# Kernel optimization log

Hardware: AMD Instinct MI355X
Metric: run time of the kernel (lower is better)

The kernel has to match this reference:

```python
import jax, jax.numpy as jnp
import numpy as np

D_MODEL = 1024

def setup_inputs() -> dict:
    key = jax.random.key(0)
    ks = jax.random.split(key, 7)
    B, S, D = 4, 2048, D_MODEL
    scale = 1.0 / np.sqrt(D)
    x = jax.random.normal(ks[0], (B, S, D), dtype=jnp.float32)
    Wq = jax.random.normal(ks[1], (D, D), dtype=jnp.float32) * scale
    bq = jnp.zeros((D,), dtype=jnp.float32)
    Wk = jax.random.normal(ks[2], (D, D), dtype=jnp.float32) * scale
    bk = jnp.zeros((D,), dtype=jnp.float32)
    Wv = jax.random.normal(ks[3], (D, D), dtype=jnp.float32) * scale
    bv = jnp.zeros((D,), dtype=jnp.float32)
    return {"x": x, "Wq": Wq, "bq": bq, "Wk": Wk, "bk": bk, "Wv": Wv, "bv": bv}

def reference(x, Wq, bq, Wk, bk, Wv, bv):
    # Single-head attention; scale = 1/sqrt(d_model) as in the torch module (self.d_k = d_model).
    d_k = x.shape[-1]
    q = jnp.einsum('bsd,de->bse', x, Wq) + bq
    k = jnp.einsum('bsd,de->bse', x, Wk) + bk
    v = jnp.einsum('bsd,de->bse', x, Wv) + bv
    scores = jnp.einsum('bqd,bkd->bqk', q, k) / jnp.sqrt(jnp.asarray(d_k, x.dtype))
    attn = jax.nn.softmax(scores, axis=-1)
    return jnp.einsum('bqk,bkd->bqd', attn, v)
```

## Files before the change

kernel.cpp:

```cpp
#include <hip/hip_runtime.h>
#include <hip/hip_bf16.h>

#define DM 1024
#define SEQ 2048
#define NBATCH 4

using f32x4 = __attribute__((ext_vector_type(4))) float;
using s16x8 = __attribute__((ext_vector_type(8))) short;
using u16x4 = __attribute__((ext_vector_type(4))) unsigned short;
using u16x8 = __attribute__((ext_vector_type(8))) unsigned short;

__device__ __forceinline__ unsigned short f2bf(float f) {
  union { float f; unsigned u; } v; v.f = f;
  return (unsigned short)((v.u + 0x7fffu + ((v.u >> 16) & 1u)) >> 16);
}

__global__ void prep_k(const float* __restrict__ X,
                       const float* __restrict__ Wq, const float* __restrict__ Wk,
                       const float* __restrict__ Wv,
                       unsigned short* __restrict__ XB, unsigned short* __restrict__ WT) {
  __shared__ float t[32][33];
  const int b = blockIdx.x;
  if (b < 4096) {
    const int i = b * 256 + threadIdx.x;
    const f32x4* p = (const f32x4*)X;
    f32x4 a = p[2 * i], c = p[2 * i + 1];
    u16x8 o;
#pragma unroll
    for (int q = 0; q < 4; q++) { o[q] = f2bf(a[q]); o[4 + q] = f2bf(c[q]); }
    *(u16x8*)(XB + (size_t)i * 8) = o;
  } else {
    const int r2 = b - 4096;
    const int seg = r2 >> 10;
    const int rem = r2 & 1023;
    const int k0 = (rem >> 5) * 32, n0 = (rem & 31) * 32;
    const float* W = (seg == 0) ? Wq : (seg == 1) ? Wk : Wv;
    unsigned short* out = WT + (size_t)seg * DM * DM;
    const int tr = threadIdx.x >> 5, tc = threadIdx.x & 31;
#pragma unroll
    for (int p = 0; p < 4; p++) {
      int r = tr + p * 8;
      t[r][tc] = W[(size_t)(k0 + r) * DM + n0 + tc];
    }
    __syncthreads();
#pragma unroll
    for (int p = 0; p < 4; p++) {
      int r = tr + p * 8;
      out[(size_t)(n0 + r) * DM + k0 + tc] = f2bf(t[tc][r]);
    }
  }
}

template <int MODE, int BM, int LDA, int LDB, int KDIM>
__global__ void gemm_nt(const unsigned short* __restrict__ A,
                        const unsigned short* __restrict__ B,
                        void* __restrict__ C0,
                        unsigned short* __restrict__ C1,
                        unsigned short* __restrict__ C2,
                        const float* __restrict__ bq,
                        const float* __restrict__ bk,
                        const float* __restrict__ bv,
                        float* __restrict__ sm,
                        float* __restrict__ sv,
                        const float* __restrict__ Tt) {
  constexpr int ASTEPS = BM / 32;
  constexpr int NJ = (BM == 128) ? 4 : 2;
  constexpr int WNOFF = 16 * NJ;
  __shared__ unsigned short lbuf[(BM + 128) * 64];
  __shared__ float fred[256];
  __shared__ float Tl[(MODE == 2) ? 1024 : 1];

  const int tid = threadIdx.x;
  const int w = tid >> 6;
  const int L = tid & 63;
  const int wm = (BM == 128) ? (w & 1) : 0;
  const int wn = (BM == 128) ? (w >> 1) : w;
  const int qd = L >> 4, ll = L & 15;

  const int bid = blockIdx.x;
  const int xcd = bid & 7, slot = bid >> 3;
  int bz, tileM, tileN, nT;
  if (MODE == 0) {
    const int pm = xcd & 3, pn = xcd >> 2;
    const int nloc = slot % 12, mloc = slot / 12;
    bz = 0; tileM = (pm * 16 + mloc) * 128; tileN = (pn * 12 + nloc) * 128; nT = 0;
  } else if (MODE == 1) {
    bz = xcd >> 1;
    const int mh = xcd & 1;
    const int nloc = slot & 15, mloc = slot >> 4;
    tileM = (mh * 8 + mloc) * 128; tileN = nloc * 128; nT = nloc;
  } else {
    bz = xcd >> 1;
    const int mh = xcd & 1;
    const int nloc = slot & 7, mloc = slot >> 3;
    tileM = (mh * 16 + mloc) * 64; tileN = nloc * 128; nT = nloc;
  }
  (void)nT;

  const unsigned short* Ab = A;
  const unsigned short* Bb = B;
  if (MODE == 1) { Ab += (size_t)bz * SEQ * DM; Bb += (size_t)bz * SEQ * DM; }
  if (MODE == 2) { Ab += (size_t)bz * SEQ * SEQ; Bb += (size_t)bz * DM * SEQ; }

  const int srow = tid >> 3;
  const int pch = tid & 7;
  const int gch = pch ^ (srow & 7);
  const unsigned short* gA = Ab + (size_t)(tileM + srow) * LDA + gch * 8;
  const unsigned short* gB = Bb + (size_t)(tileN + srow) * LDB + gch * 8;
  unsigned short* lA = lbuf;
  unsigned short* lB = lbuf + BM * 64;
  unsigned short* wAp = &lA[srow * 64 + pch * 8];
  unsigned short* wBp = &lB[srow * 64 + pch * 8];

  u16x8 rA[ASTEPS], rB[4];
#define LOADT(kt) do {                                                         \
    const size_t kk_ = (size_t)(kt) * 64;                                      \
    _Pragma("unroll")                                                          \
    for (int i_ = 0; i_ < ASTEPS; i_++)                                        \
      rA[i_] = *(const u16x8*)(gA + (size_t)i_ * 32 * LDA + kk_);              \
    _Pragma("unroll")                                                          \
    for (int i_ = 0; i_ < 4; i_++)                                             \
      rB[i_] = *(const u16x8*)(gB + (size_t)i_ * 32 * LDB + kk_);              \
  } while (0)
#define WRITET() do {                                                          \
    _Pragma("unroll")                                                          \
    for (int i_ = 0; i_ < ASTEPS; i_++) *(u16x8*)(wAp + i_ * 32 * 64) = rA[i_];\
    _Pragma("unroll")                                                          \
    for (int i_ = 0; i_ < 4; i_++)      *(u16x8*)(wBp + i_ * 32 * 64) = rB[i_];\
  } while (0)

  f32x4 acc[4][NJ];
#pragma unroll
  for (int i = 0; i < 4; i++)
#pragma unroll
    for (int j = 0; j < NJ; j++) acc[i][j] = (f32x4){0.f, 0.f, 0.f, 0.f};

  const int sw = L & 7;

  constexpr int NK = KDIM / 64;
  LOADT(0);

  if (MODE == 2 && tid < 64) {
    const size_t rbase = (size_t)bz * SEQ + tileM + tid;
    const float* mrow = sm + rbase * 16;
    const float* srow2 = sv + rbase * 32;
    float mv[16];
#pragma unroll
    for (int t = 0; t < 16; t++) mv[t] = mrow[t];
    float M = mv[0];
#pragma unroll
    for (int t = 1; t < 16; t++) M = fmaxf(M, mv[t]);
    float Lsum = 0.f;
#pragma unroll
    for (int t = 0; t < 16; t++) Lsum += (srow2[2 * t] + srow2[2 * t + 1]) * __expf(mv[t] - M);
#pragma unroll
    for (int t = 1; t < 16; t++) Tl[(t - 1) * 64 + tid] = __expf(mv[t - 1] - mv[t]);
    Tl[15 * 64 + tid] = __expf(mv[15] - M) / Lsum;
  }

  WRITET();
  __syncthreads();

  float tTn[4][4];
  if (MODE == 2) {
#pragma unroll
    for (int i = 0; i < 4; i++)
#pragma unroll
      for (int r = 0; r < 4; r++) tTn[i][r] = Tl[i * 16 + qd * 4 + r];
  }

  for (int k = 0; k < NK; ++k) {
    if (MODE == 2 && k >= 2 && (k & 1) == 0) {
#pragma unroll
      for (int i = 0; i < 4; i++)
#pragma unroll
        for (int j = 0; j < NJ; j++)
#pragma unroll
          for (int r = 0; r < 4; r++) acc[i][j][r] *= tTn[i][r];
      const int tn = (k >> 1) + 1;
#pragma unroll
      for (int i = 0; i < 4; i++)
#pragma unroll
        for (int r = 0; r < 4; r++) tTn[i][r] = Tl[(tn - 1) * 64 + i * 16 + qd * 4 + r];
    }

    if (k + 1 < NK) LOADT(k + 1);

#pragma unroll
    for (int s = 0; s < 2; s++) {
      const int pc = ((s * 4 + qd) ^ sw) * 8;
      s16x8 av[4], bv4[NJ];
#pragma unroll
      for (int i = 0; i < 4; i++)
        av[i] = *(const s16x8*)&lA[(wm * 64 + i * 16 + ll) * 64 + pc];
#pragma unroll
      for (int j = 0; j < NJ; j++)
        bv4[j] = *(const s16x8*)&lB[(wn * WNOFF + j * 16 + ll) * 64 + pc];
#pragma unroll
      for (int i = 0; i < 4; i++)
#pragma unroll
        for (int j = 0; j < NJ; j++)
          acc[i][j] = __builtin_amdgcn_mfma_f32_16x16x32_bf16(av[i], bv4[j], acc[i][j], 0, 0, 0);
    }

    if (k + 1 < NK) {
      __builtin_amdgcn_s_waitcnt(0xC07F);
      __builtin_amdgcn_sched_barrier(0);
      __builtin_amdgcn_s_barrier();
      __builtin_amdgcn_sched_barrier(0);
      WRITET();
      __syncthreads();
    }
  }
#undef LOADT
#undef WRITET

  if (MODE == 0) {
#pragma unroll
    for (int i = 0; i < 4; i++) {
      const int gm0 = tileM + wm * 64 + i * 16 + qd * 4;
#pragma unroll
      for (int j = 0; j < NJ; j++) {
        const int gn = tileN + wn * WNOFF + j * 16 + ll;
        const int seg = gn >> 10;
        const int colin = gn & 1023;
        if (seg == 0) {
          const float bias = bq[colin];
          unsigned short* Q = (unsigned short*)C0;
#pragma unroll
          for (int r = 0; r < 4; r++) Q[(size_t)(gm0 + r) * DM + colin] = f2bf(acc[i][j][r] + bias);
        } else if (seg == 1) {
          const float bias = bk[colin];
#pragma unroll
          for (int r = 0; r < 4; r++) C1[(size_t)(gm0 + r) * DM + colin] = f2bf(acc[i][j][r] + bias);
        } else {
          const float bias = bv[colin];
          u16x4 pk;
#pragma unroll
          for (int r = 0; r < 4; r++) pk[r] = f2bf(acc[i][j][r] + bias);
          const int b = gm0 >> 11, s0 = gm0 & 2047;
          *(u16x4*)(C2 + ((size_t)((b << 10) + colin)) * SEQ + s0) = pk;
        }
      }
    }
  } else if (MODE == 1) {
    __syncthreads();
    float mt[4][4];
#pragma unroll
    for (int i = 0; i < 4; i++)
#pragma unroll
      for (int r = 0; r < 4; r++) {
#pragma unroll
        for (int j = 0; j < NJ; j++) acc[i][j][r] *= 0.03125f;
        float v = fmaxf(fmaxf(acc[i][0][r], acc[i][1][r]), fmaxf(acc[i][2][r], acc[i][3][r]));
#pragma unroll
        for (int m = 1; m < 16; m <<= 1) v = fmaxf(v, __shfl_xor(v, m, 16));
        mt[i][r] = v;
      }
    if (ll == 0) {
#pragma unroll
      for (int i = 0; i < 4; i++)
#pragma unroll
        for (int r = 0; r < 4; r++)
          fred[wn * 128 + wm * 64 + i * 16 + qd * 4 + r] = mt[i][r];
    }
    __syncthreads();
#pragma unroll
    for (int i = 0; i < 4; i++)
#pragma unroll
      for (int r = 0; r < 4; r++) {
        const int row = wm * 64 + i * 16 + qd * 4 + r;
        mt[i][r] = fmaxf(fred[row], fred[128 + row]);
      }
#pragma unroll
    for (int i = 0; i < 4; i++)
#pragma unroll
      for (int r = 0; r < 4; r++) {
        const int row = wm * 64 + i * 16 + qd * 4 + r;
        float s = 0.f;
#pragma unroll
        for (int j = 0; j < NJ; j++) {
          float e = __expf(acc[i][j][r] - mt[i][r]);
          s += e;
          const int col = wn * WNOFF + j * 16 + ll;
          lbuf[row * 128 + ((((col >> 4) ^ (row & 7)) << 4) | (col & 15))] = f2bf(e);
        }
#pragma unroll
        for (int m = 1; m < 16; m <<= 1) s += __shfl_xor(s, m, 16);
        if (ll == 0) {
          const size_t base = (size_t)bz * SEQ + tileM + row;
          sv[base * 32 + nT * 2 + wn] = s;
          if (wn == 0) sm[base * 16 + nT] = mt[i][r];
        }
      }
    __syncthreads();
    unsigned short* P = (unsigned short*)C0 + (size_t)bz * SEQ * SEQ;
#pragma unroll
    for (int p = 0; p < 8; p++) {
      const int c = p * 256 + tid;
      const int row = c >> 4, cg = c & 15;
      const int phys = ((((cg >> 1) ^ (row & 7)) << 4) | ((cg & 1) << 3));
      u16x8 val = *(const u16x8*)&lbuf[row * 128 + phys];
      *(u16x8*)(P + (size_t)(tileM + row) * SEQ + tileN + cg * 8) = val;
    }
  } else {
    float* O = (float*)C0 + (size_t)bz * SEQ * DM;
#pragma unroll
    for (int i = 0; i < 4; i++) {
      const int gm0 = tileM + i * 16 + qd * 4;
#pragma unroll
      for (int j = 0; j < NJ; j++) {
        const int gn = tileN + wn * WNOFF + j * 16 + ll;
#pragma unroll
        for (int r = 0; r < 4; r++)
          O[(size_t)(gm0 + r) * DM + gn] = acc[i][j][r] * tTn[i][r];
      }
    }
  }
  (void)Tt;
}

extern "C" void kernel_launch(void* const* d_in, const int* in_sizes, int n_in,
                              void* d_out, int out_size, void* d_ws, size_t ws_size,
                              hipStream_t stream) {
  (void)in_sizes; (void)n_in; (void)out_size; (void)ws_size;
  const float* x  = (const float*)d_in[0];
  const float* Wq = (const float*)d_in[1];
  const float* bq = (const float*)d_in[2];
  const float* Wk = (const float*)d_in[3];
  const float* bk = (const float*)d_in[4];
  const float* Wv = (const float*)d_in[5];
  const float* bv = (const float*)d_in[6];
  float* out = (float*)d_out;
  char* ws = (char*)d_ws;
  unsigned short* xb = (unsigned short*)(ws + 0);
  unsigned short* wt = (unsigned short*)(ws + 16777216);
  unsigned short* qb = (unsigned short*)(ws + 23068672);
  unsigned short* kb = (unsigned short*)(ws + 39845888);
  unsigned short* vt = (unsigned short*)(ws + 56623104);
  unsigned short* P  = (unsigned short*)(ws + 73400320);
  float*          ms = (float*)(ws + 106954752);
  float*          ss = (float*)(ws + 107479040);

  prep_k<<<7168, 256, 0, stream>>>(x, Wq, Wk, Wv, xb, wt);
  gemm_nt<0, 128, 1024, 1024, 1024><<<1536, 256, 0, stream>>>(
      xb, wt, (void*)qb, kb, vt, bq, bk, bv, nullptr, nullptr, nullptr);
  gemm_nt<1, 128, 1024, 1024, 1024><<<1024, 256, 0, stream>>>(
      qb, kb, (void*)P, nullptr, nullptr, nullptr, nullptr, nullptr, ms, ss, nullptr);
  gemm_nt<2, 64, 2048, 2048, 2048><<<1024, 256, 0, stream>>>(
      P, vt, (void*)out, nullptr, nullptr, nullptr, nullptr, nullptr, ms, ss, nullptr);
}
```

Before: 253.1 us.

## Replace QK^T scores GEMM with 256x256-tile kernel using direct global-to-LDS loads

Adds a dedicated scores kernel with 256x256 output tiles and 8 waves. It stages Q/K tiles straight into LDS via global_load_lds in a double-buffered pipeline with explicit barriers, waitcnts and priority hints. The per-tile softmax statistics change from 16 to 8 column tiles, and the PV GEMM's rescale schedule is updated to match. The aim is more data reuse per tile and overlap of loads with MFMA work, but there are only 256 blocks and P is now written with scattered 2-byte stores instead of staged vector stores.

```diff
diff --git a/kernel.cpp b/kernel.cpp
--- a/kernel.cpp
+++ b/kernel.cpp
@@ -13,6 +13,12 @@
 __device__ __forceinline__ unsigned short f2bf(float f) {
   union { float f; unsigned u; } v; v.f = f;
   return (unsigned short)((v.u + 0x7fffu + ((v.u >> 16) & 1u)) >> 16);
+}
+
+__device__ __forceinline__ void gll16(const unsigned short* g, unsigned short* l) {
+  __builtin_amdgcn_global_load_lds((const __attribute__((address_space(1))) void*)g,
+                                   (__attribute__((address_space(3))) void*)l,
+                                   16, 0, 0);
 }
 
 __global__ void prep_k(const float* __restrict__ X,
@@ -49,6 +55,171 @@
       out[(size_t)(n0 + r) * DM + k0 + tc] = f2bf(t[tc][r]);
     }
   }
+}
+
+__global__ __launch_bounds__(512, 2) void sgemm256_k(
+    const unsigned short* __restrict__ Qb,
+    const unsigned short* __restrict__ Kb,
+    unsigned short* __restrict__ P,
+    float* __restrict__ sm,
+    float* __restrict__ sv) {
+  __shared__ unsigned short lbuf[65536];
+  __shared__ float fred[1024];
+
+  const int tid = threadIdx.x;
+  const int w = tid >> 6, l = tid & 63;
+  const int ll = l & 15, qd = l >> 4;
+  const int wm = w >> 2, wn = w & 3;
+
+  const int bid = blockIdx.x;
+  const int xcd = bid & 7, slot = bid >> 3;
+  const int bz = xcd >> 1;
+  const int mh = xcd & 1;
+  const int nloc = slot & 7, mloc = slot >> 3;
+  const int tileM = (mh * 4 + mloc) * 256, tileN = nloc * 256;
+  const int nT = nloc;
+
+  const int seg = l >> 3, ch = l & 7;
+  const int rowo = seg * 2 + (ch >> 2);
+  const int kc = (ch & 3) ^ (seg & 3);
+  const unsigned short* gA0 = Qb + (size_t)(bz * SEQ + tileM + w * 16 + rowo) * DM + kc * 8;
+  const unsigned short* gB0 = Kb + (size_t)(bz * SEQ + tileN + w * 16 + rowo) * DM + kc * 8;
+
+#define STG_A(bsel, t_, ks_) do {                                              \
+    unsigned short* d_ = lbuf + (bsel) * 16384 + (ks_) * 8192 + w * 512;       \
+    const unsigned short* s_ = gA0 + (t_) * 64 + (ks_) * 32;                   \
+    gll16(s_, d_); gll16(s_ + 128 * DM, d_ + 4096); } while (0)
+#define STG_B(bsel, t_, ks_) do {                                              \
+    unsigned short* d_ = lbuf + 32768 + (bsel) * 16384 + (ks_) * 8192 + w * 512; \
+    const unsigned short* s_ = gB0 + (t_) * 64 + (ks_) * 32;                   \
+    gll16(s_, d_); gll16(s_ + 128 * DM, d_ + 4096); } while (0)
+
+  const int Ra = wm * 128 + ll;
+  const int aoff0 = (Ra >> 1) * 64 + (((Ra & 1) << 2) + (qd ^ ((Ra >> 1) & 3))) * 8;
+  const int Rb = wn * 64 + ll;
+  const int boff0 = (Rb >> 1) * 64 + (((Rb & 1) << 2) + (qd ^ ((Rb >> 1) & 3))) * 8;
+
+  f32x4 acc[8][4];
+#pragma unroll
+  for (int i = 0; i < 8; i++)
+#pragma unroll
+    for (int j = 0; j < 4; j++) acc[i][j] = (f32x4){0.f, 0.f, 0.f, 0.f};
+  s16x8 bfr[4];
+
+#define PH(bsel, ks_, ih_, DOSTG, DOVM, VMC) do {                              \
+    const int ab_ = (bsel) * 16384 + (ks_) * 8192;                             \
+    s16x8 af_[4];                                                              \
+    _Pragma("unroll")                                                          \
+    for (int i_ = 0; i_ < 4; i_++)                                             \
+      af_[i_] = *(const s16x8*)&lbuf[ab_ + aoff0 + ((ih_) * 4 + i_) * 512];    \
+    if (!(ih_)) {                                                              \
+      _Pragma("unroll")                                                        \
+      for (int j_ = 0; j_ < 4; j_++)                                           \
+        bfr[j_] = *(const s16x8*)&lbuf[32768 + ab_ + boff0 + j_ * 512];        \
+    }                                                                          \
+    DOSTG;                                                                     \
+    __builtin_amdgcn_sched_barrier(0);                                         \
+    if (DOVM) { __builtin_amdgcn_s_waitcnt(VMC);                               \
+                __builtin_amdgcn_sched_barrier(0); }                           \
+    __builtin_amdgcn_s_barrier();                                              \
+    __builtin_amdgcn_s_waitcnt(0xC07F);                        \
+    __builtin_amdgcn_sched_barrier(0);                                         \
+    __builtin_amdgcn_s_setprio(1);                                             \
+    _Pragma("unroll")                                                          \
+    for (int i_ = 0; i_ < 4; i_++)                                             \
+      _Pragma("unroll")                                                        \
+      for (int j_ = 0; j_ < 4; j_++)                                           \
+        acc[(ih_) * 4 + i_][j_] = __builtin_amdgcn_mfma_f32_16x16x32_bf16(     \
+            af_[i_], bfr[j_], acc[(ih_) * 4 + i_][j_], 0, 0, 0);               \
+    __builtin_amdgcn_s_setprio(0);                                             \
+    __builtin_amdgcn_sched_barrier(0);                                         \
+    __builtin_amdgcn_s_barrier();                                              \
+    __builtin_amdgcn_sched_barrier(0);                                         \
+  } while (0)
+
+  STG_A(0, 0, 0); STG_A(0, 0, 1); STG_B(0, 0, 0); STG_B(0, 0, 1);
+  STG_A(1, 1, 0); STG_B(1, 1, 0);
+  __builtin_amdgcn_sched_barrier(0);
+  __builtin_amdgcn_s_waitcnt(0x0F74);
+  __builtin_amdgcn_sched_barrier(0);
+  __builtin_amdgcn_s_barrier();
+  __builtin_amdgcn_sched_barrier(0);
+
+#define TILE_STEADY(bsel, t_) do {                                             \
+    PH(bsel, 0, 0, STG_A(1 - (bsel), (t_) + 1, 1), 0, 0);                      \
+    PH(bsel, 0, 1, STG_B(1 - (bsel), (t_) + 1, 1), 1, 0x0F78);                 \
+    PH(bsel, 1, 0, STG_A(bsel, (t_) + 2, 0), 0, 0);                            \
+    PH(bsel, 1, 1, STG_B(bsel, (t_) + 2, 0), 1, 0x0F78);                       \
+  } while (0)
+
+  for (int I = 0; I < 7; ++I) {
+    const int t = 2 * I;
+    TILE_STEADY(0, t);
+    TILE_STEADY(1, t + 1);
+  }
+  PH(0, 0, 0, STG_A(1, 15, 1), 0, 0);
+  PH(0, 0, 1, STG_B(1, 15, 1), 1, 0x0F78);
+  PH(0, 1, 0, (void)0, 0, 0);
+  PH(0, 1, 1, (void)0, 1, 0x0F74);
+  PH(1, 0, 0, (void)0, 0, 0);
+  PH(1, 0, 1, (void)0, 1, 0x0F70);
+  PH(1, 1, 0, (void)0, 0, 0);
+  PH(1, 1, 1, (void)0, 0, 0);
+#undef TILE_STEADY
+#undef PH
+#undef STG_A
+#undef STG_B
+
+  float mt[8][4];
+#pragma unroll
+  for (int i = 0; i < 8; i++)
+#pragma unroll
+    for (int r = 0; r < 4; r++) {
+#pragma unroll
+      for (int j = 0; j < 4; j++) acc[i][j][r] *= 0.03125f;
+      float v = fmaxf(fmaxf(acc[i][0][r], acc[i][1][r]), fmaxf(acc[i][2][r], acc[i][3][r]));
+#pragma unroll
+      for (int m = 1; m < 16; m <<= 1) v = fmaxf(v, __shfl_xor(v, m, 16));
+      mt[i][r] = v;
+    }
+  if (ll == 0) {
+#pragma unroll
+    for (int i = 0; i < 8; i++)
+#pragma unroll
+      for (int r = 0; r < 4; r++)
+        fred[wn * 256 + wm * 128 + i * 16 + qd * 4 + r] = mt[i][r];
+  }
+  __syncthreads();
+#pragma unroll
+  for (int i = 0; i < 8; i++)
+#pragma unroll
+    for (int r = 0; r < 4; r++) {
+      const int row = wm * 128 + i * 16 + qd * 4 + r;
+      mt[i][r] = fmaxf(fmaxf(fred[row], fred[256 + row]),
+                       fmaxf(fred[512 + row], fred[768 + row]));
+    }
+  unsigned short* Pb = P + (size_t)bz * SEQ * SEQ;
+#pragma unroll
+  for (int i = 0; i < 8; i++)
+#pragma unroll
+    for (int r = 0; r < 4; r++) {
+      const int row = wm * 128 + i * 16 + qd * 4 + r;
+      const int rowg = tileM + row;
+      float s = 0.f;
+#pragma unroll
+      for (int j = 0; j < 4; j++) {
+        const float e = __expf(acc[i][j][r] - mt[i][r]);
+        s += e;
+        Pb[(size_t)rowg * SEQ + tileN + wn * 64 + j * 16 + ll] = f2bf(e);
+      }
+#pragma unroll
+      for (int m = 1; m < 16; m <<= 1) s += __shfl_xor(s, m, 16);
+      if (ll == 0) {
+        const size_t base = (size_t)bz * SEQ + rowg;
+        sv[base * 32 + nT * 4 + wn] = s;
+        if (wn == 0) sm[base * 8 + nT] = mt[i][r];
+      }
+    }
 }
 
 template <int MODE, int BM, int LDA, int LDB, int KDIM>
@@ -67,8 +238,7 @@
   constexpr int NJ = (BM == 128) ? 4 : 2;
   constexpr int WNOFF = 16 * NJ;
   __shared__ unsigned short lbuf[(BM + 128) * 64];
-  __shared__ float fred[256];
-  __shared__ float Tl[(MODE == 2) ? 1024 : 1];
+  __shared__ float Tl[(MODE == 2) ? 512 : 1];
 
   const int tid = threadIdx.x;
   const int w = tid >> 6;
@@ -79,27 +249,20 @@
 
   const int bid = blockIdx.x;
   const int xcd = bid & 7, slot = bid >> 3;
-  int bz, tileM, tileN, nT;
+  int bz, tileM, tileN;
   if (MODE == 0) {
     const int pm = xcd & 3, pn = xcd >> 2;
     const int nloc = slot % 12, mloc = slot / 12;
-    bz = 0; tileM = (pm * 16 + mloc) * 128; tileN = (pn * 12 + nloc) * 128; nT = 0;
-  } else if (MODE == 1) {
-    bz = xcd >> 1;
-    const int mh = xcd & 1;
-    const int nloc = slot & 15, mloc = slot >> 4;
-    tileM = (mh * 8 + mloc) * 128; tileN = nloc * 128; nT = nloc;
+    bz = 0; tileM = (pm * 16 + mloc) * 128; tileN = (pn * 12 + nloc) * 128;
   } else {
     bz = xcd >> 1;
     const int mh = xcd & 1;
     const int nloc = slot & 7, mloc = slot >> 3;
-    tileM = (mh * 16 + mloc) * 64; tileN = nloc * 128; nT = nloc;
-  }
-  (void)nT;
+    tileM = (mh * 16 + mloc) * 64; tileN = nloc * 128;
+  }
 
   const unsigned short* Ab = A;
   const unsigned short* Bb = B;
-  if (MODE == 1) { Ab += (size_t)bz * SEQ * DM; Bb += (size_t)bz * SEQ * DM; }
   if (MODE == 2) { Ab += (size_t)bz * SEQ * SEQ; Bb += (size_t)bz * DM * SEQ; }
 
   const int srow = tid >> 3;
@@ -142,20 +305,22 @@
 
   if (MODE == 2 && tid < 64) {
     const size_t rbase = (size_t)bz * SEQ + tileM + tid;
-    const float* mrow = sm + rbase * 16;
+    const float* mrow = sm + rbase * 8;
     const float* srow2 = sv + rbase * 32;
-    float mv[16];
-#pragma unroll
-    for (int t = 0; t < 16; t++) mv[t] = mrow[t];
+    float mv[8];
+#pragma unroll
+    for (int t = 0; t < 8; t++) mv[t] = mrow[t];
     float M = mv[0];
 #pragma unroll
-    for (int t = 1; t < 16; t++) M = fmaxf(M, mv[t]);
+    for (int t = 1; t < 8; t++) M = fmaxf(M, mv[t]);
     float Lsum = 0.f;
 #pragma unroll
-    for (int t = 0; t < 16; t++) Lsum += (srow2[2 * t] + srow2[2 * t + 1]) * __expf(mv[t] - M);
-#pragma unroll
-    for (int t = 1; t < 16; t++) Tl[(t - 1) * 64 + tid] = __expf(mv[t - 1] - mv[t]);
-    Tl[15 * 64 + tid] = __expf(mv[15] - M) / Lsum;
+    for (int t = 0; t < 8; t++)
+      Lsum += (srow2[4 * t] + srow2[4 * t + 1] + srow2[4 * t + 2] + srow2[4 * t + 3]) *
+              __expf(mv[t] - M);
+#pragma unroll
+    for (int t = 1; t < 8; t++) Tl[(t - 1) * 64 + tid] = __expf(mv[t - 1] - mv[t]);
+    Tl[7 * 64 + tid] = __expf(mv[7] - M) / Lsum;
   }
 
   WRITET();
@@ -170,18 +335,18 @@
   }
 
   for (int k = 0; k < NK; ++k) {
-    if (MODE == 2 && k >= 2 && (k & 1) == 0) {
+    if (MODE == 2 && k >= 4 && (k & 3) == 0) {
 #pragma unroll
       for (int i = 0; i < 4; i++)
 #pragma unroll
         for (int j = 0; j < NJ; j++)
 #pragma unroll
           for (int r = 0; r < 4; r++) acc[i][j][r] *= tTn[i][r];
-      const int tn = (k >> 1) + 1;
+      const int tn1 = (k >> 2);
 #pragma unroll
       for (int i = 0; i < 4; i++)
 #pragma unroll
-        for (int r = 0; r < 4; r++) tTn[i][r] = Tl[(tn - 1) * 64 + i * 16 + qd * 4 + r];
+        for (int r = 0; r < 4; r++) tTn[i][r] = Tl[tn1 * 64 + i * 16 + qd * 4 + r];
     }
 
     if (k + 1 < NK) LOADT(k + 1);
@@ -243,66 +408,6 @@
         }
       }
     }
-  } else if (MODE == 1) {
-    __syncthreads();
-    float mt[4][4];
-#pragma unroll
-    for (int i = 0; i < 4; i++)
-#pragma unroll
-      for (int r = 0; r < 4; r++) {
-#pragma unroll
-        for (int j = 0; j < NJ; j++) acc[i][j][r] *= 0.03125f;
-        float v = fmaxf(fmaxf(acc[i][0][r], acc[i][1][r]), fmaxf(acc[i][2][r], acc[i][3][r]));
-#pragma unroll
-        for (int m = 1; m < 16; m <<= 1) v = fmaxf(v, __shfl_xor(v, m, 16));
-        mt[i][r] = v;
-      }
-    if (ll == 0) {
-#pragma unroll
-      for (int i = 0; i < 4; i++)
-#pragma unroll
-        for (int r = 0; r < 4; r++)
-          fred[wn * 128 + wm * 64 + i * 16 + qd * 4 + r] = mt[i][r];
-    }
-    __syncthreads();
-#pragma unroll
-    for (int i = 0; i < 4; i++)
-#pragma unroll
-      for (int r = 0; r < 4; r++) {
-        const int row = wm * 64 + i * 16 + qd * 4 + r;
-        mt[i][r] = fmaxf(fred[row], fred[128 + row]);
-      }
-#pragma unroll
-    for (int i = 0; i < 4; i++)
-#pragma unroll
-      for (int r = 0; r < 4; r++) {
-        const int row = wm * 64 + i * 16 + qd * 4 + r;
-        float s = 0.f;
-#pragma unroll
-        for (int j = 0; j < NJ; j++) {
-          float e = __expf(acc[i][j][r] - mt[i][r]);
-          s += e;
-          const int col = wn * WNOFF + j * 16 + ll;
-          lbuf[row * 128 + ((((col >> 4) ^ (row & 7)) << 4) | (col & 15))] = f2bf(e);
-        }
-#pragma unroll
-        for (int m = 1; m < 16; m <<= 1) s += __shfl_xor(s, m, 16);
-        if (ll == 0) {
-          const size_t base = (size_t)bz * SEQ + tileM + row;
-          sv[base * 32 + nT * 2 + wn] = s;
-          if (wn == 0) sm[base * 16 + nT] = mt[i][r];
-        }
-      }
-    __syncthreads();
-    unsigned short* P = (unsigned short*)C0 + (size_t)bz * SEQ * SEQ;
-#pragma unroll
-    for (int p = 0; p < 8; p++) {
-      const int c = p * 256 + tid;
-      const int row = c >> 4, cg = c & 15;
-      const int phys = ((((cg >> 1) ^ (row & 7)) << 4) | ((cg & 1) << 3));
-      u16x8 val = *(const u16x8*)&lbuf[row * 128 + phys];
-      *(u16x8*)(P + (size_t)(tileM + row) * SEQ + tileN + cg * 8) = val;
-    }
   } else {
     float* O = (float*)C0 + (size_t)bz * SEQ * DM;
 #pragma unroll
@@ -317,7 +422,7 @@
       }
     }
   }
-  (void)Tt;
+  (void)sm; (void)sv; (void)Tt;
 }
 
 extern "C" void kernel_launch(void* const* d_in, const int* in_sizes, int n_in,
@@ -345,8 +450,7 @@
   prep_k<<<7168, 256, 0, stream>>>(x, Wq, Wk, Wv, xb, wt);
   gemm_nt<0, 128, 1024, 1024, 1024><<<1536, 256, 0, stream>>>(
       xb, wt, (void*)qb, kb, vt, bq, bk, bv, nullptr, nullptr, nullptr);
-  gemm_nt<1, 128, 1024, 1024, 1024><<<1024, 256, 0, stream>>>(
-      qb, kb, (void*)P, nullptr, nullptr, nullptr, nullptr, nullptr, ms, ss, nullptr);
+  sgemm256_k<<<256, 512, 0, stream>>>(qb, kb, P, ms, ss);
   gemm_nt<2, 64, 2048, 2048, 2048><<<1024, 256, 0, stream>>>(
       P, vt, (void*)out, nullptr, nullptr, nullptr, nullptr, nullptr, ms, ss, nullptr);
 }
```

Result: slower. 261.2 us (+3.2%).
